# Optimization experiments

Hardware: AMD Instinct MI355X
Metric: run time of the kernel (lower is better)

The kernel has to match this reference:

```python
import jax, jax.numpy as jnp
import numpy as np
import math

B, T, IN, H, OUT, L = 8, 256, 128, 128, 128, 2
MAX_EP_LEN = 10000.0


def _rotate(x, pos, d):
    # rope as in source: repeat(1,1,2) = concat along last dim (not interleave)
    half = jnp.exp(jnp.arange(0, d, 2, dtype=jnp.float32) * (-math.log(MAX_EP_LEN) / d))  # [d/2]
    ang = pos[..., None] * half  # [B,T,d/2]
    sine = jnp.concatenate([jnp.sin(ang), jnp.sin(ang)], axis=-1)
    cos = jnp.concatenate([jnp.cos(ang), jnp.cos(ang)], axis=-1)
    y1, y2 = jnp.split(x, 2, axis=-1)
    x_rot = jnp.concatenate([-y2, y1], axis=-1)
    return x * cos + x_rot * sine


def _layernorm(x, w, b, eps=1e-5):
    m = jnp.mean(x, axis=-1, keepdims=True)
    v = jnp.mean((x - m) ** 2, axis=-1, keepdims=True)
    return (x - m) / jnp.sqrt(v + eps) * w + b


def _block(x, S0, Z0, Wk, Wq, Wv, lw, lb, w1, b1, w2, b2, scw, scb):
    # x: [B,T,F]; S0: [B,F,F]; Z0: [B,F]
    x = _layernorm(x, lw, lb)
    K = jax.nn.elu(x @ Wk.T) + 1.0
    Q = jax.nn.elu(x @ Wq.T) + 1.0
    V = x @ Wv.T
    outer = jnp.einsum('bti,btj->btij', K, V)  # [B,T,F,F]
    S = jnp.clip(jnp.cumsum(outer, axis=1), -1e20, 1e20) + S0[:, None]  # [B,T,F,F]
    Z = jnp.clip(jnp.cumsum(K, axis=1), -1e20, 1e20) + Z0[:, None]      # [B,T,F]
    num = jnp.einsum('bti,btil->btl', Q, S)
    den = jnp.einsum('bti,bti->bt', Q, Z)[..., None] + 1e-5
    out = num / den
    out = jax.nn.relu(jax.nn.relu(out @ w1.T + b1) @ w2.T + b2)  # feed_forward
    out = out + x @ scw.T + scb                                   # residual shortcut
    return out, S[:, -1], Z[:, -1]


def setup_inputs() -> dict:
    key = jax.random.key(0)
    ks = jax.random.split(key, 14)
    s = 0.05
    return {
        'z': jax.random.normal(ks[0], (T, B, IN), jnp.float32),
        'state': jnp.zeros((B, L * (H * H + H) + 1), jnp.float32),
        'Wk': jax.random.normal(ks[1], (L, H, IN), jnp.float32) * s,
        'Wq': jax.random.normal(ks[2], (L, H, IN), jnp.float32) * s,
        'Wv': jax.random.normal(ks[3], (L, H, IN), jnp.float32) * s,
        'ln_w': jnp.ones((L, IN), jnp.float32),
        'ln_b': jnp.zeros((L, IN), jnp.float32),
        'ff_w1': jax.random.normal(ks[4], (L, H, H), jnp.float32) * s,
        'ff_b1': jnp.zeros((L, H), jnp.float32),
        'ff_w2': jax.random.normal(ks[5], (L, H, H), jnp.float32) * s,
        'ff_b2': jnp.zeros((L, H), jnp.float32),
        'sc_w': jax.random.normal(ks[6], (L, H, IN), jnp.float32) * s,
        'sc_b': jnp.zeros((L, H), jnp.float32),
        'unmap_w': jax.random.normal(ks[7], (OUT, H), jnp.float32) * s,
        'unmap_b': jnp.zeros((OUT,), jnp.float32),
    }


def reference(z, state, Wk, Wq, Wv, ln_w, ln_b, ff_w1, ff_b1, ff_w2, ff_b2, sc_w, sc_b, unmap_w, unmap_b):
    x = jnp.transpose(z, (1, 0, 2))  # [B,T,IN]
    ts = state[:, -1]                # [B] timestep counters
    core = state[:, :-1].reshape(B, L, H * H + H)
    pos = ts[:, None] + jnp.arange(T, dtype=jnp.float32)[None, :]  # [B,T]
    x = _rotate(x, pos, IN)  # embedding_type == 'rope'
    new_states = []
    for i in range(L):
        S0 = core[:, i, :H * H].reshape(B, H, H)
        Z0 = core[:, i, H * H:]
        x, Sl, Zl = _block(x, S0, Z0, Wk[i], Wq[i], Wv[i], ln_w[i], ln_b[i],
                           ff_w1[i], ff_b1[i], ff_w2[i], ff_b2[i], sc_w[i], sc_b[i])
        new_states.append(jnp.concatenate([Sl.reshape(B, -1), Zl], axis=-1))
    y = x @ unmap_w.T + unmap_b
    st = jnp.concatenate([jnp.stack(new_states, axis=1).reshape(B, -1), (ts + T)[:, None]], axis=-1)
    return jnp.transpose(y, (1, 0, 2)), st
```

## Files before the change

### kernel.cpp

```cpp
#include <hip/hip_runtime.h>
#include <math.h>

#define Bn 8
#define Tn 256
#define COREn 16512
#define SDn   33025

typedef __attribute__((ext_vector_type(8))) short short8;
typedef __attribute__((ext_vector_type(4))) short short4v;
typedef __attribute__((ext_vector_type(4))) float floatx4;

#define MFMA16(a,b,c) __builtin_amdgcn_mfma_f32_16x16x32_bf16(a,b,c,0,0,0)

static __device__ __forceinline__ unsigned short f2bf(float f) {
  unsigned int u = __float_as_uint(f);
  return (unsigned short)((u + 0x7FFFu + ((u >> 16) & 1u)) >> 16);
}
static __device__ __forceinline__ float bf2f(unsigned short h) {
  return __uint_as_float((unsigned int)h << 16);
}
static __device__ __forceinline__ short8 ldwfrag(const float* p) {
  float4 a = *(const float4*)p;
  float4 b = *(const float4*)(p + 4);
  short8 r;
  r[0] = (short)f2bf(a.x); r[1] = (short)f2bf(a.y);
  r[2] = (short)f2bf(a.z); r[3] = (short)f2bf(a.w);
  r[4] = (short)f2bf(b.x); r[5] = (short)f2bf(b.y);
  r[6] = (short)f2bf(b.z); r[7] = (short)f2bf(b.w);
  return r;
}
static __device__ __forceinline__ void ld8(const float* p, float* v) {
  float4 a = *(const float4*)p, b = *(const float4*)(p + 4);
  v[0]=a.x; v[1]=a.y; v[2]=a.z; v[3]=a.w; v[4]=b.x; v[5]=b.y; v[6]=b.z; v[7]=b.w;
}

static __device__ __forceinline__ void proj_epilogue(
    int by, int g0, int b, int t0l, int n0, int n1, int quad,
    floatx4 acc0, floatx4 acc1,
    unsigned short* __restrict__ Kb, unsigned short* __restrict__ Kt,
    unsigned short* __restrict__ Qb, unsigned short* __restrict__ Vt,
    unsigned short* __restrict__ skipb, const float* __restrict__ scb) {
  if (by == 0) {
    short4v kt0, kt1;
#pragma unroll
    for (int j = 0; j < 4; j++) {
      int row = quad * 4 + j;
      float e0 = acc0[j] > 0.f ? acc0[j] + 1.f : expf(acc0[j]);
      float e1 = acc1[j] > 0.f ? acc1[j] + 1.f : expf(acc1[j]);
      Kb[(size_t)(g0 + row) * 128 + n0] = f2bf(e0);
      Kb[(size_t)(g0 + row) * 128 + n1] = f2bf(e1);
      kt0[j] = (short)f2bf(e0); kt1[j] = (short)f2bf(e1);
    }
    *(short4v*)(Kt + (size_t)(b * 128 + n0) * 256 + t0l + quad * 4) = kt0;
    *(short4v*)(Kt + (size_t)(b * 128 + n1) * 256 + t0l + quad * 4) = kt1;
  } else if (by == 1) {
#pragma unroll
    for (int j = 0; j < 4; j++) {
      int row = quad * 4 + j;
      float e0 = acc0[j] > 0.f ? acc0[j] + 1.f : expf(acc0[j]);
      float e1 = acc1[j] > 0.f ? acc1[j] + 1.f : expf(acc1[j]);
      Qb[(size_t)(g0 + row) * 128 + n0] = f2bf(e0);
      Qb[(size_t)(g0 + row) * 128 + n1] = f2bf(e1);
    }
  } else if (by == 2) {
    short4v v0, v1;
#pragma unroll
    for (int j = 0; j < 4; j++) { v0[j] = (short)f2bf(acc0[j]); v1[j] = (short)f2bf(acc1[j]); }
    *(short4v*)(Vt + (size_t)(b * 128 + n0) * 256 + t0l + quad * 4) = v0;
    *(short4v*)(Vt + (size_t)(b * 128 + n1) * 256 + t0l + quad * 4) = v1;
  } else {
    float sb0 = scb[n0], sb1 = scb[n1];
#pragma unroll
    for (int j = 0; j < 4; j++) {
      int row = quad * 4 + j;
      skipb[(size_t)(g0 + row) * 128 + n0] = f2bf(acc0[j] + sb0);
      skipb[(size_t)(g0 + row) * 128 + n1] = f2bf(acc1[j] + sb1);
    }
  }
}

__global__ __launch_bounds__(256) void prep_kernel(
    const float* __restrict__ z, const float* __restrict__ state,
    const float* __restrict__ Wk, const float* __restrict__ Wq,
    const float* __restrict__ Wv, const float* __restrict__ scw,
    const float* __restrict__ lnw, const float* __restrict__ lnb,
    const float* __restrict__ scb,
    unsigned short* __restrict__ Kb0, unsigned short* __restrict__ Qb0,
    unsigned short* __restrict__ Kt0, unsigned short* __restrict__ Vt0,
    unsigned short* __restrict__ skip0, unsigned short* __restrict__ S0t) {
  const int tid = threadIdx.x, bx = blockIdx.x;
  if (bx < 512) {
    __shared__ unsigned short xs[16][136];
    const int lane = tid & 63, wv = tid >> 6, lm = lane & 15, quad = lane >> 4;
    const int tile = bx >> 2, by = bx & 3;
    const int g0 = tile * 16;
    const int r = tid >> 4, c0 = (tid & 15) * 8;
    const int g = g0 + r, b = g >> 8, t = g & 255;
    float v[8], pv[8];
    const float* zr = z + ((size_t)t * Bn + b) * 128;
    ld8(zr + c0, v);
    ld8(zr + (c0 ^ 64), pv);
    float pos = state[(size_t)b * SDn + SDn - 1] + (float)t;
#pragma unroll
    for (int i = 0; i < 8; i++) {
      int jj = (c0 + i) & 63;
      float ang = pos * expf((float)jj * -0.14391156831212787f);
      float sn = sinf(ang), cs = cosf(ang);
      v[i] = (c0 < 64) ? (v[i] * cs - pv[i] * sn) : (v[i] * cs + pv[i] * sn);
    }
    float sm = 0.f, sq = 0.f;
#pragma unroll
    for (int i = 0; i < 8; i++) { sm += v[i]; sq += v[i] * v[i]; }
    for (int d = 8; d; d >>= 1) { sm += __shfl_xor(sm, d, 16); sq += __shfl_xor(sq, d, 16); }
    float mean = sm * (1.f / 128.f);
    float rstd = rsqrtf(sq * (1.f / 128.f) - mean * mean + 1e-5f);
    short8 xv;
#pragma unroll
    for (int i = 0; i < 8; i++)
      xv[i] = (short)f2bf((v[i] - mean) * rstd * lnw[c0 + i] + lnb[c0 + i]);
    *(short8*)&xs[r][c0] = xv;
    __syncthreads();

    const float* W = by == 0 ? Wk : by == 1 ? Wq : by == 2 ? Wv : scw;
    const int bb = g0 >> 8, t0l = g0 & 255;
    const int n0 = wv * 32 + lm, n1 = n0 + 16;
    floatx4 a0 = {0.f,0.f,0.f,0.f}, a1 = {0.f,0.f,0.f,0.f};
#pragma unroll
    for (int kc = 0; kc < 4; kc++) {
      short8 a  = *(const short8*)&xs[lm][kc * 32 + quad * 8];
      short8 bA = ldwfrag(W + (size_t)n0 * 128 + kc * 32 + quad * 8);
      short8 bB = ldwfrag(W + (size_t)n1 * 128 + kc * 32 + quad * 8);
      a0 = MFMA16(a, bA, a0);
      a1 = MFMA16(a, bB, a1);
    }
    proj_epilogue(by, g0, bb, t0l, n0, n1, quad, a0, a1,
                  Kb0, Kt0, Qb0, Vt0, skip0, scb);
  } else {
    __shared__ float tl[32][33];
    const int id = bx - 512, b = id >> 1, l = id & 1;
    const float* src = state + (size_t)b * SDn + (size_t)l * COREn;
    unsigned short* dst = S0t + (size_t)(l * 8 + b) * 16384;
    const int r = tid >> 3, c4 = (tid & 7) * 4;
#pragma unroll
    for (int tI = 0; tI < 4; tI++)
      for (int tJ = 0; tJ < 4; tJ++) {
        int i0 = tI * 32, j0 = tJ * 32;
#pragma unroll
        for (int q = 0; q < 4; q++)
          tl[r][c4 + q] = src[(size_t)(i0 + r) * 128 + j0 + c4 + q];
        __syncthreads();
        short4v o;
#pragma unroll
        for (int q = 0; q < 4; q++) o[q] = (short)f2bf(tl[c4 + q][r]);
        *(short4v*)(dst + (size_t)(j0 + r) * 128 + i0 + c4) = o;
        __syncthreads();
      }
  }
}

static __device__ void state_upd(
    int tid, int idx, int l,
    const unsigned short* __restrict__ Kt, const unsigned short* __restrict__ Vt,
    const float* __restrict__ state, float* __restrict__ st_out) {
  const int lane = tid & 63, wv = tid >> 6, lm = lane & 15, quad = lane >> 4;
  const int b = idx >> 4, sub = idx & 15;
  const int i0 = (sub >> 1) * 16, j0 = (sub & 1) * 64;
  const size_t sb = (size_t)b * SDn + (size_t)l * COREn;
  floatx4 acc = {0.f, 0.f, 0.f, 0.f};
#pragma unroll
  for (int kc = 0; kc < 8; kc++) {
    short8 ka = *(const short8*)(Kt + (size_t)(b * 128 + i0 + lm) * 256 + kc * 32 + quad * 8);
    short8 vb = *(const short8*)(Vt + (size_t)(b * 128 + j0 + wv * 16 + lm) * 256 + kc * 32 + quad * 8);
    acc = MFMA16(ka, vb, acc);
  }
#pragma unroll
  for (int j = 0; j < 4; j++) {
    size_t off = sb + (size_t)(i0 + quad * 4 + j) * 128 + j0 + wv * 16 + lm;
    st_out[off] = acc[j] + state[off];
  }
  if (j0 == 0) {
    if (tid < 128) {
      int i = tid >> 3, seg = tid & 7;
      const unsigned short* kr = Kt + (size_t)(b * 128 + i0 + i) * 256 + seg * 32;
      float zs = 0.f;
#pragma unroll
      for (int x = 0; x < 4; x++) {
        short8 kv = *(const short8*)(kr + x * 8);
#pragma unroll
        for (int y = 0; y < 8; y++) zs += bf2f((unsigned short)kv[y]);
      }
      for (int d = 4; d; d >>= 1) zs += __shfl_xor(zs, d, 8);
      if (seg == 0) {
        size_t zo = sb + 16384 + i0 + i;
        st_out[zo] = zs + state[zo];
      }
    }
    if (sub == 0 && tid == 0 && l == 0)
      st_out[(size_t)b * SDn + SDn - 1] = state[(size_t)b * SDn + SDn - 1] + 256.f;
  }
}

__global__ __launch_bounds__(256) void attn_kernel(
    const unsigned short* __restrict__ Kb, const unsigned short* __restrict__ Qb,
    const unsigned short* __restrict__ Vt, const unsigned short* __restrict__ Kt,
    const unsigned short* __restrict__ S0tl, const float* __restrict__ state,
    unsigned short* __restrict__ attnb, float* __restrict__ st_out, int l) {
  const int tid = threadIdx.x, bx = blockIdx.x;
  const int lane = tid & 63, wv = tid >> 6, lm = lane & 15, quad = lane >> 4;
  if (bx < 256) {
    __shared__ unsigned short xs[16][136];
    __shared__ unsigned short Ssc[4][16][40];
    __shared__ float Obuf[4][16][68];
    __shared__ float Z0s[128];
    __shared__ float denw[4][16];
    __shared__ float denz[16];
    __shared__ float dinv[16];

    const int tile = bx >> 1, half = bx & 1;
    const int b = tile >> 4, rt = tile & 15, t0 = rt * 16;
    const size_t sb = (size_t)b * SDn + (size_t)l * COREn;
    { int r = tid >> 4, c = (tid & 15) * 8;
      *(short8*)&xs[r][c] = *(const short8*)(Qb + (size_t)(b * 256 + t0 + r) * 128 + c); }
    if (tid < 128) Z0s[tid] = state[sb + 16384 + tid];
    __syncthreads();

    { int r = tid >> 4, c = (tid & 15) * 8;
      float qz = 0.f;
#pragma unroll
      for (int i = 0; i < 8; i++) qz += bf2f(xs[r][c + i]) * Z0s[c + i];
      for (int d = 8; d; d >>= 1) qz += __shfl_xor(qz, d, 16);
      if ((tid & 15) == 0) denz[r] = qz; }

    floatx4 oacc[4];
#pragma unroll
    for (int jt = 0; jt < 4; jt++) oacc[jt] = floatx4{0.f, 0.f, 0.f, 0.f};
    float dacc[4] = {0.f, 0.f, 0.f, 0.f};

    const int nch = rt / 2 + 1;
    for (int c = wv; c < nch; c += 4) {
      const int kb = c * 32;
      short8 vfr[4];
#pragma unroll
      for (int jt = 0; jt < 4; jt++)
        vfr[jt] = *(const short8*)(Vt + (size_t)(b * 128 + half * 64 + jt * 16 + lm) * 256 + kb + quad * 8);
      floatx4 s0 = {0.f,0.f,0.f,0.f}, s1 = {0.f,0.f,0.f,0.f};
#pragma unroll
      for (int kc = 0; kc < 4; kc++) {
        short8 a  = *(const short8*)&xs[lm][kc * 32 + quad * 8];
        short8 k0 = *(const short8*)(Kb + (size_t)(b * 256 + kb + lm) * 128 + kc * 32 + quad * 8);
        short8 k1 = *(const short8*)(Kb + (size_t)(b * 256 + kb + 16 + lm) * 128 + kc * 32 + quad * 8);
        s0 = MFMA16(a, k0, s0);
        s1 = MFMA16(a, k1, s1);
      }
      const int tau0 = kb + lm, tau1 = kb + 16 + lm;
#pragma unroll
      for (int j = 0; j < 4; j++) {
        int m = t0 + quad * 4 + j;
        float v0 = (tau0 <= m) ? s0[j] : 0.f;
        float v1 = (tau1 <= m) ? s1[j] : 0.f;
        dacc[j] += v0 + v1;
        Ssc[wv][quad * 4 + j][lm]      = f2bf(v0);
        Ssc[wv][quad * 4 + j][16 + lm] = f2bf(v1);
      }
      short8 sa = *(const short8*)&Ssc[wv][lm][quad * 8];
#pragma unroll
      for (int jt = 0; jt < 4; jt++)
        oacc[jt] = MFMA16(sa, vfr[jt], oacc[jt]);
    }

    { short8 aq = *(const short8*)&xs[lm][wv * 32 + quad * 8];
#pragma unroll
      for (int jt = 0; jt < 4; jt++) {
        short8 vb = *(const short8*)(S0tl + (size_t)b * 16384 +
                        (size_t)(half * 64 + jt * 16 + lm) * 128 + wv * 32 + quad * 8);
        oacc[jt] = MFMA16(aq, vb, oacc[jt]);
      } }

#pragma unroll
    for (int j = 0; j < 4; j++)
      for (int d = 8; d; d >>= 1) dacc[j] += __shfl_xor(dacc[j], d, 16);
    if (lm == 0) {
#pragma unroll
      for (int j = 0; j < 4; j++) denw[wv][quad * 4 + j] = dacc[j];
    }
#pragma unroll
    for (int jt = 0; jt < 4; jt++)
#pragma unroll
      for (int j = 0; j < 4; j++)
        Obuf[wv][quad * 4 + j][jt * 16 + lm] = oacc[jt][j];
    __syncthreads();
    if (tid < 16)
      dinv[tid] = 1.f / (denz[tid] + denw[0][tid] + denw[1][tid]
                         + denw[2][tid] + denw[3][tid] + 1e-5f);
    __syncthreads();
    { int r = tid >> 4, c = (tid & 15) * 4;
      float di = dinv[r];
      short4v ov;
#pragma unroll
      for (int q = 0; q < 4; q++) {
        float o = Obuf[0][r][c + q] + Obuf[1][r][c + q]
                + Obuf[2][r][c + q] + Obuf[3][r][c + q];
        ov[q] = (short)f2bf(o * di);
      }
      *(short4v*)(attnb + (size_t)(b * 256 + t0 + r) * 128 + half * 64 + c) = ov; }
  } else {
    state_upd(tid, bx - 256, l, Kt, Vt, state, st_out);
  }
}

__global__ __launch_bounds__(256) void ffln_kernel(
    const unsigned short* __restrict__ attnb, const unsigned short* __restrict__ skipb,
    const float* __restrict__ w1, const float* __restrict__ b1,
    const float* __restrict__ w2, const float* __restrict__ b2,
    const float* __restrict__ lnw1, const float* __restrict__ lnb1,
    unsigned short* __restrict__ xln1) {
  __shared__ unsigned short xa[16][136];
  __shared__ unsigned short hs[16][136];
  __shared__ float os[16][132];
  const int tid = threadIdx.x, g0 = blockIdx.x * 16;
  const int lane = tid & 63, wv = tid >> 6, lm = lane & 15, quad = lane >> 4;
  const int n0 = wv * 32 + lm, n1 = n0 + 16;

  short8 w1A[4], w1B[4], w2A[4], w2B[4];
#pragma unroll
  for (int kc = 0; kc < 4; kc++) {
    w1A[kc] = ldwfrag(w1 + (size_t)n0 * 128 + kc * 32 + quad * 8);
    w1B[kc] = ldwfrag(w1 + (size_t)n1 * 128 + kc * 32 + quad * 8);
    w2A[kc] = ldwfrag(w2 + (size_t)n0 * 128 + kc * 32 + quad * 8);
    w2B[kc] = ldwfrag(w2 + (size_t)n1 * 128 + kc * 32 + quad * 8);
  }
  float bi10 = b1[n0], bi11 = b1[n1], bi20 = b2[n0], bi21 = b2[n1];
  float sk0[4], sk1[4];
#pragma unroll
  for (int j = 0; j < 4; j++) {
    sk0[j] = bf2f(skipb[(size_t)(g0 + quad * 4 + j) * 128 + n0]);
    sk1[j] = bf2f(skipb[(size_t)(g0 + quad * 4 + j) * 128 + n1]);
  }
  { int r = tid >> 4, c = (tid & 15) * 8;
    *(short8*)&xa[r][c] = *(const short8*)(attnb + (size_t)(g0 + r) * 128 + c); }
  __syncthreads();

  { floatx4 a0 = {0.f,0.f,0.f,0.f}, a1 = {0.f,0.f,0.f,0.f};
#pragma unroll
    for (int kc = 0; kc < 4; kc++) {
      short8 a = *(const short8*)&xa[lm][kc * 32 + quad * 8];
      a0 = MFMA16(a, w1A[kc], a0);
      a1 = MFMA16(a, w1B[kc], a1);
    }
#pragma unroll
    for (int j = 0; j < 4; j++) {
      int row = quad * 4 + j;
      hs[row][n0] = f2bf(fmaxf(a0[j] + bi10, 0.f));
      hs[row][n1] = f2bf(fmaxf(a1[j] + bi11, 0.f));
    } }
  __syncthreads();
  { floatx4 a0 = {0.f,0.f,0.f,0.f}, a1 = {0.f,0.f,0.f,0.f};
#pragma unroll
    for (int kc = 0; kc < 4; kc++) {
      short8 a = *(const short8*)&hs[lm][kc * 32 + quad * 8];
      a0 = MFMA16(a, w2A[kc], a0);
      a1 = MFMA16(a, w2B[kc], a1);
    }
#pragma unroll
    for (int j = 0; j < 4; j++) {
      int row = quad * 4 + j;
      os[row][n0] = fmaxf(a0[j] + bi20, 0.f) + sk0[j];
      os[row][n1] = fmaxf(a1[j] + bi21, 0.f) + sk1[j];
    } }
  __syncthreads();
  { int r = tid >> 4, c0 = (tid & 15) * 8;
    float v[8];
#pragma unroll
    for (int i = 0; i < 8; i++) v[i] = os[r][c0 + i];
    float sm = 0.f, sq = 0.f;
#pragma unroll
    for (int i = 0; i < 8; i++) { sm += v[i]; sq += v[i] * v[i]; }
    for (int d = 8; d; d >>= 1) { sm += __shfl_xor(sm, d, 16); sq += __shfl_xor(sq, d, 16); }
    float mean = sm * (1.f / 128.f);
    float rstd = rsqrtf(sq * (1.f / 128.f) - mean * mean + 1e-5f);
    short8 xv;
#pragma unroll
    for (int i = 0; i < 8; i++)
      xv[i] = (short)f2bf((v[i] - mean) * rstd * lnw1[c0 + i] + lnb1[c0 + i]);
    *(short8*)(xln1 + (size_t)(g0 + r) * 128 + c0) = xv; }
}

__global__ __launch_bounds__(256) void proj1_kernel(
    const unsigned short* __restrict__ xln1,
    const float* __restrict__ Wk, const float* __restrict__ Wq,
    const float* __restrict__ Wv, const float* __restrict__ scw,
    const float* __restrict__ scb,
    unsigned short* __restrict__ Kb1, unsigned short* __restrict__ Qb1,
    unsigned short* __restrict__ Kt1, unsigned short* __restrict__ Vt1,
    unsigned short* __restrict__ skip1) {
  __shared__ unsigned short xs[16][136];
  const int tid = threadIdx.x, bx = blockIdx.x;
  const int lane = tid & 63, wv = tid >> 6, lm = lane & 15, quad = lane >> 4;
  const int tile = bx >> 2, by = bx & 3;
  const int g0 = tile * 16;
  { int r = tid >> 4, c = (tid & 15) * 8;
    *(short8*)&xs[r][c] = *(const short8*)(xln1 + (size_t)(g0 + r) * 128 + c); }
  __syncthreads();
  const float* W = by == 0 ? Wk : by == 1 ? Wq : by == 2 ? Wv : scw;
  const int bb = g0 >> 8, t0l = g0 & 255;
  const int n0 = wv * 32 + lm, n1 = n0 + 16;
  floatx4 a0 = {0.f,0.f,0.f,0.f}, a1 = {0.f,0.f,0.f,0.f};
#pragma unroll
  for (int kc = 0; kc < 4; kc++) {
    short8 a  = *(const short8*)&xs[lm][kc * 32 + quad * 8];
    short8 bA = ldwfrag(W + (size_t)n0 * 128 + kc * 32 + quad * 8);
    short8 bB = ldwfrag(W + (size_t)n1 * 128 + kc * 32 + quad * 8);
    a0 = MFMA16(a, bA, a0);
    a1 = MFMA16(a, bB, a1);
  }
  proj_epilogue(by, g0, bb, t0l, n0, n1, quad, a0, a1,
                Kb1, Kt1, Qb1, Vt1, skip1, scb);
}

__global__ __launch_bounds__(256) void ffu_kernel(
    const unsigned short* __restrict__ attnb, const unsigned short* __restrict__ skipb,
    const float* __restrict__ w1, const float* __restrict__ b1,
    const float* __restrict__ w2, const float* __restrict__ b2,
    const float* __restrict__ unw, const float* __restrict__ unb,
    float* __restrict__ yout) {
  __shared__ unsigned short xa[16][136];
  __shared__ unsigned short hs[16][136];
  const int tid = threadIdx.x, g0 = blockIdx.x * 16;
  const int lane = tid & 63, wv = tid >> 6, lm = lane & 15, quad = lane >> 4;
  const int n0 = wv * 32 + lm, n1 = n0 + 16;

  short8 w1A[4], w1B[4], w2A[4], w2B[4];
#pragma unroll
  for (int kc = 0; kc < 4; kc++) {
    w1A[kc] = ldwfrag(w1 + (size_t)n0 * 128 + kc * 32 + quad * 8);
    w1B[kc] = ldwfrag(w1 + (size_t)n1 * 128 + kc * 32 + quad * 8);
    w2A[kc] = ldwfrag(w2 + (size_t)n0 * 128 + kc * 32 + quad * 8);
    w2B[kc] = ldwfrag(w2 + (size_t)n1 * 128 + kc * 32 + quad * 8);
  }
  float bi10 = b1[n0], bi11 = b1[n1], bi20 = b2[n0], bi21 = b2[n1];
  float sk0[4], sk1[4];
#pragma unroll
  for (int j = 0; j < 4; j++) {
    sk0[j] = bf2f(skipb[(size_t)(g0 + quad * 4 + j) * 128 + n0]);
    sk1[j] = bf2f(skipb[(size_t)(g0 + quad * 4 + j) * 128 + n1]);
  }
  { int r = tid >> 4, c = (tid & 15) * 8;
    *(short8*)&xa[r][c] = *(const short8*)(attnb + (size_t)(g0 + r) * 128 + c); }
  __syncthreads();

  { floatx4 a0 = {0.f,0.f,0.f,0.f}, a1 = {0.f,0.f,0.f,0.f};
#pragma unroll
    for (int kc = 0; kc < 4; kc++) {
      short8 a = *(const short8*)&xa[lm][kc * 32 + quad * 8];
      a0 = MFMA16(a, w1A[kc], a0);
      a1 = MFMA16(a, w1B[kc], a1);
    }
#pragma unroll
    for (int j = 0; j < 4; j++) {
      int row = quad * 4 + j;
      hs[row][n0] = f2bf(fmaxf(a0[j] + bi10, 0.f));
      hs[row][n1] = f2bf(fmaxf(a1[j] + bi11, 0.f));
    } }
  __syncthreads();
  short8 uA[4], uB[4];
#pragma unroll
  for (int kc = 0; kc < 4; kc++) {
    uA[kc] = ldwfrag(unw + (size_t)n0 * 128 + kc * 32 + quad * 8);
    uB[kc] = ldwfrag(unw + (size_t)n1 * 128 + kc * 32 + quad * 8);
  }
  float o0[4], o1[4];
  { floatx4 a0 = {0.f,0.f,0.f,0.f}, a1 = {0.f,0.f,0.f,0.f};
#pragma unroll
    for (int kc = 0; kc < 4; kc++) {
      short8 a = *(const short8*)&hs[lm][kc * 32 + quad * 8];
      a0 = MFMA16(a, w2A[kc], a0);
      a1 = MFMA16(a, w2B[kc], a1);
    }
#pragma unroll
    for (int j = 0; j < 4; j++) {
      o0[j] = fmaxf(a0[j] + bi20, 0.f) + sk0[j];
      o1[j] = fmaxf(a1[j] + bi21, 0.f) + sk1[j];
    } }
  __syncthreads();
#pragma unroll
  for (int j = 0; j < 4; j++) {
    int row = quad * 4 + j;
    hs[row][n0] = f2bf(o0[j]);
    hs[row][n1] = f2bf(o1[j]);
  }
  __syncthreads();
  { floatx4 a0 = {0.f,0.f,0.f,0.f}, a1 = {0.f,0.f,0.f,0.f};
#pragma unroll
    for (int kc = 0; kc < 4; kc++) {
      short8 a = *(const short8*)&hs[lm][kc * 32 + quad * 8];
      a0 = MFMA16(a, uA[kc], a0);
      a1 = MFMA16(a, uB[kc], a1);
    }
    float u0 = unb[n0], u1 = unb[n1];
#pragma unroll
    for (int j = 0; j < 4; j++) {
      int gg = g0 + quad * 4 + j;
      int bb = gg >> 8, tq = gg & 255;
      yout[(size_t)(tq * Bn + bb) * 128 + n0] = a0[j] + u0;
      yout[(size_t)(tq * Bn + bb) * 128 + n1] = a1[j] + u1;
    } }
}

extern "C" void kernel_launch(void* const* d_in, const int* in_sizes, int n_in,
                              void* d_out, int out_size, void* d_ws, size_t ws_size,
                              hipStream_t stream) {
  const float* z       = (const float*)d_in[0];
  const float* state   = (const float*)d_in[1];
  const float* Wk      = (const float*)d_in[2];
  const float* Wq      = (const float*)d_in[3];
  const float* Wv      = (const float*)d_in[4];
  const float* ln_w    = (const float*)d_in[5];
  const float* ln_b    = (const float*)d_in[6];
  const float* ff_w1   = (const float*)d_in[7];
  const float* ff_b1   = (const float*)d_in[8];
  const float* ff_w2   = (const float*)d_in[9];
  const float* ff_b2   = (const float*)d_in[10];
  const float* sc_w    = (const float*)d_in[11];
  const float* sc_b    = (const float*)d_in[12];
  const float* unmap_w = (const float*)d_in[13];
  const float* unmap_b = (const float*)d_in[14];

  float* y_out  = (float*)d_out;
  float* st_out = y_out + (size_t)Tn * Bn * 128;

  const size_t E = 262144;
  unsigned short* Kb0  = (unsigned short*)d_ws;
  unsigned short* Qb0  = Kb0 + E;
  unsigned short* Kt0  = Qb0 + E;
  unsigned short* Vt0  = Kt0 + E;
  unsigned short* Kb1  = Vt0 + E;
  unsigned short* Qb1  = Kb1 + E;
  unsigned short* Kt1  = Qb1 + E;
  unsigned short* Vt1  = Kt1 + E;
  unsigned short* skip0 = Vt1 + E;
  unsigned short* skip1 = skip0 + E;
  unsigned short* attnb = skip1 + E;
  unsigned short* xln1  = attnb + E;
  unsigned short* S0t   = xln1 + E;

  prep_kernel<<<528, 256, 0, stream>>>(
      z, state, Wk, Wq, Wv, sc_w, ln_w, ln_b, sc_b,
      Kb0, Qb0, Kt0, Vt0, skip0, S0t);

  attn_kernel<<<384, 256, 0, stream>>>(
      Kb0, Qb0, Vt0, Kt0, S0t, state, attnb, st_out, 0);

  ffln_kernel<<<128, 256, 0, stream>>>(
      attnb, skip0, ff_w1, ff_b1, ff_w2, ff_b2,
      ln_w + 128, ln_b + 128, xln1);

  proj1_kernel<<<512, 256, 0, stream>>>(
      xln1, Wk + 16384, Wq + 16384, Wv + 16384, sc_w + 16384, sc_b + 128,
      Kb1, Qb1, Kt1, Vt1, skip1);

  attn_kernel<<<384, 256, 0, stream>>>(
      Kb1, Qb1, Vt1, Kt1, S0t + (size_t)8 * 16384, state, attnb, st_out, 1);

  ffu_kernel<<<128, 256, 0, stream>>>(
      attnb, skip1, ff_w1 + 16384, ff_b1 + 128, ff_w2 + 16384, ff_b2 + 128,
      unmap_w, unmap_b, y_out);
}
```

Baseline: 130.4 us.

## Fuse FF/LN with layer-1 projection, hoist loads, and prewarm weights in L2

Merges the ffln and proj1 kernels into a single ffproj kernel. The layer-1 LayerNorm output now stays in shared memory instead of round-tripping through a global xln1 buffer, and one launch is removed. The attention, prep and state-update kernels issue all K/V/S0/weight fragment loads up front into registers so memory latency overlaps with compute. The attention loop is unrolled to two fixed chunks per wave. Extra prep blocks read the layer-1 and FF weights to warm the L2 cache, and launch_bounds(256,1) is added; in exchange ffproj has only 128 blocks doing four projections each, which lowers parallelism, and register use rises.

```diff
diff --git a/kernel.cpp b/kernel.cpp
--- a/kernel.cpp
+++ b/kernel.cpp
@@ -79,15 +79,18 @@
   }
 }
 
-__global__ __launch_bounds__(256) void prep_kernel(
+__global__ __launch_bounds__(256, 1) void prep_kernel(
     const float* __restrict__ z, const float* __restrict__ state,
     const float* __restrict__ Wk, const float* __restrict__ Wq,
     const float* __restrict__ Wv, const float* __restrict__ scw,
     const float* __restrict__ lnw, const float* __restrict__ lnb,
     const float* __restrict__ scb,
+    const float* __restrict__ w1all, const float* __restrict__ w2all,
+    const float* __restrict__ unw,
     unsigned short* __restrict__ Kb0, unsigned short* __restrict__ Qb0,
     unsigned short* __restrict__ Kt0, unsigned short* __restrict__ Vt0,
-    unsigned short* __restrict__ skip0, unsigned short* __restrict__ S0t) {
+    unsigned short* __restrict__ skip0, unsigned short* __restrict__ S0t,
+    float* __restrict__ warm_sink) {
   const int tid = threadIdx.x, bx = blockIdx.x;
   if (bx < 512) {
     __shared__ unsigned short xs[16][136];
@@ -96,11 +99,21 @@
     const int g0 = tile * 16;
     const int r = tid >> 4, c0 = (tid & 15) * 8;
     const int g = g0 + r, b = g >> 8, t = g & 255;
+    const int n0 = wv * 32 + lm, n1 = n0 + 16;
+
     float v[8], pv[8];
     const float* zr = z + ((size_t)t * Bn + b) * 128;
     ld8(zr + c0, v);
     ld8(zr + (c0 ^ 64), pv);
+    const float* W = by == 0 ? Wk : by == 1 ? Wq : by == 2 ? Wv : scw;
+    short8 bA[4], bB[4];
+#pragma unroll
+    for (int kc = 0; kc < 4; kc++) {
+      bA[kc] = ldwfrag(W + (size_t)n0 * 128 + kc * 32 + quad * 8);
+      bB[kc] = ldwfrag(W + (size_t)n1 * 128 + kc * 32 + quad * 8);
+    }
     float pos = state[(size_t)b * SDn + SDn - 1] + (float)t;
+
 #pragma unroll
     for (int i = 0; i < 8; i++) {
       int jj = (c0 + i) & 63;
@@ -121,21 +134,17 @@
     *(short8*)&xs[r][c0] = xv;
     __syncthreads();
 
-    const float* W = by == 0 ? Wk : by == 1 ? Wq : by == 2 ? Wv : scw;
     const int bb = g0 >> 8, t0l = g0 & 255;
-    const int n0 = wv * 32 + lm, n1 = n0 + 16;
     floatx4 a0 = {0.f,0.f,0.f,0.f}, a1 = {0.f,0.f,0.f,0.f};
 #pragma unroll
     for (int kc = 0; kc < 4; kc++) {
-      short8 a  = *(const short8*)&xs[lm][kc * 32 + quad * 8];
-      short8 bA = ldwfrag(W + (size_t)n0 * 128 + kc * 32 + quad * 8);
-      short8 bB = ldwfrag(W + (size_t)n1 * 128 + kc * 32 + quad * 8);
-      a0 = MFMA16(a, bA, a0);
-      a1 = MFMA16(a, bB, a1);
+      short8 a = *(const short8*)&xs[lm][kc * 32 + quad * 8];
+      a0 = MFMA16(a, bA[kc], a0);
+      a1 = MFMA16(a, bB[kc], a1);
     }
     proj_epilogue(by, g0, bb, t0l, n0, n1, quad, a0, a1,
                   Kb0, Kt0, Qb0, Vt0, skip0, scb);
-  } else {
+  } else if (bx < 528) {
     __shared__ float tl[32][33];
     const int id = bx - 512, b = id >> 1, l = id & 1;
     const float* src = state + (size_t)b * SDn + (size_t)l * COREn;
@@ -155,6 +164,17 @@
         *(short4v*)(dst + (size_t)(j0 + r) * 128 + i0 + c4) = o;
         __syncthreads();
       }
+  } else {
+    const int wb = bx - 528;
+    const float* ptrs[9] = { w1all, w1all + 16384, w2all, w2all + 16384, unw,
+                             Wk + 16384, Wq + 16384, Wv + 16384, scw + 16384 };
+    float acc = 0.f;
+#pragma unroll
+    for (int i = 0; i < 9; i++) {
+      float4 vv = ((const float4*)ptrs[i])[wb * 256 + tid];
+      acc += vv.x + vv.y + vv.z + vv.w;
+    }
+    if (acc == 1234567.89f) warm_sink[0] = acc;
   }
 }
 
@@ -166,13 +186,15 @@
   const int b = idx >> 4, sub = idx & 15;
   const int i0 = (sub >> 1) * 16, j0 = (sub & 1) * 64;
   const size_t sb = (size_t)b * SDn + (size_t)l * COREn;
+  short8 ka[8], vb[8];
+#pragma unroll
+  for (int kc = 0; kc < 8; kc++) {
+    ka[kc] = *(const short8*)(Kt + (size_t)(b * 128 + i0 + lm) * 256 + kc * 32 + quad * 8);
+    vb[kc] = *(const short8*)(Vt + (size_t)(b * 128 + j0 + wv * 16 + lm) * 256 + kc * 32 + quad * 8);
+  }
   floatx4 acc = {0.f, 0.f, 0.f, 0.f};
 #pragma unroll
-  for (int kc = 0; kc < 8; kc++) {
-    short8 ka = *(const short8*)(Kt + (size_t)(b * 128 + i0 + lm) * 256 + kc * 32 + quad * 8);
-    short8 vb = *(const short8*)(Vt + (size_t)(b * 128 + j0 + wv * 16 + lm) * 256 + kc * 32 + quad * 8);
-    acc = MFMA16(ka, vb, acc);
-  }
+  for (int kc = 0; kc < 8; kc++) acc = MFMA16(ka[kc], vb[kc], acc);
 #pragma unroll
   for (int j = 0; j < 4; j++) {
     size_t off = sb + (size_t)(i0 + quad * 4 + j) * 128 + j0 + wv * 16 + lm;
@@ -200,7 +222,7 @@
   }
 }
 
-__global__ __launch_bounds__(256) void attn_kernel(
+__global__ __launch_bounds__(256, 1) void attn_kernel(
     const unsigned short* __restrict__ Kb, const unsigned short* __restrict__ Qb,
     const unsigned short* __restrict__ Vt, const unsigned short* __restrict__ Kt,
     const unsigned short* __restrict__ S0tl, const float* __restrict__ state,
@@ -219,15 +241,38 @@
     const int tile = bx >> 1, half = bx & 1;
     const int b = tile >> 4, rt = tile & 15, t0 = rt * 16;
     const size_t sb = (size_t)b * SDn + (size_t)l * COREn;
-    { int r = tid >> 4, c = (tid & 15) * 8;
-      *(short8*)&xs[r][c] = *(const short8*)(Qb + (size_t)(b * 256 + t0 + r) * 128 + c); }
-    if (tid < 128) Z0s[tid] = state[sb + 16384 + tid];
+
+    const int r = tid >> 4, cQ = (tid & 15) * 8;
+    short8 qrow = *(const short8*)(Qb + (size_t)(b * 256 + t0 + r) * 128 + cQ);
+    float z0v = (tid < 128) ? state[sb + 16384 + tid] : 0.f;
+
+    const int nch = rt / 2 + 1;
+    const bool hasA = (wv < nch), hasB = (wv + 4 < nch);
+    const int kbA = (hasA ? wv : nch - 1) * 32;
+    const int kbB = (hasB ? wv + 4 : nch - 1) * 32;
+    short8 KA[8], KB[8], VA[4], VB[4], SF[4];
+#pragma unroll
+    for (int kc = 0; kc < 4; kc++) {
+      KA[kc]     = *(const short8*)(Kb + (size_t)(b * 256 + kbA + lm) * 128 + kc * 32 + quad * 8);
+      KA[4 + kc] = *(const short8*)(Kb + (size_t)(b * 256 + kbA + 16 + lm) * 128 + kc * 32 + quad * 8);
+      KB[kc]     = *(const short8*)(Kb + (size_t)(b * 256 + kbB + lm) * 128 + kc * 32 + quad * 8);
+      KB[4 + kc] = *(const short8*)(Kb + (size_t)(b * 256 + kbB + 16 + lm) * 128 + kc * 32 + quad * 8);
+    }
+#pragma unroll
+    for (int jt = 0; jt < 4; jt++) {
+      VA[jt] = *(const short8*)(Vt + (size_t)(b * 128 + half * 64 + jt * 16 + lm) * 256 + kbA + quad * 8);
+      VB[jt] = *(const short8*)(Vt + (size_t)(b * 128 + half * 64 + jt * 16 + lm) * 256 + kbB + quad * 8);
+      SF[jt] = *(const short8*)(S0tl + (size_t)b * 16384 +
+                    (size_t)(half * 64 + jt * 16 + lm) * 128 + wv * 32 + quad * 8);
+    }
+
+    *(short8*)&xs[r][cQ] = qrow;
+    if (tid < 128) Z0s[tid] = z0v;
     __syncthreads();
 
-    { int r = tid >> 4, c = (tid & 15) * 8;
-      float qz = 0.f;
-#pragma unroll
-      for (int i = 0; i < 8; i++) qz += bf2f(xs[r][c + i]) * Z0s[c + i];
+    { float qz = 0.f;
+#pragma unroll
+      for (int i = 0; i < 8; i++) qz += bf2f(xs[r][cQ + i]) * Z0s[cQ + i];
       for (int d = 8; d; d >>= 1) qz += __shfl_xor(qz, d, 16);
       if ((tid & 15) == 0) denz[r] = qz; }
 
@@ -236,45 +281,53 @@
     for (int jt = 0; jt < 4; jt++) oacc[jt] = floatx4{0.f, 0.f, 0.f, 0.f};
     float dacc[4] = {0.f, 0.f, 0.f, 0.f};
 
-    const int nch = rt / 2 + 1;
-    for (int c = wv; c < nch; c += 4) {
-      const int kb = c * 32;
-      short8 vfr[4];
-#pragma unroll
-      for (int jt = 0; jt < 4; jt++)
-        vfr[jt] = *(const short8*)(Vt + (size_t)(b * 128 + half * 64 + jt * 16 + lm) * 256 + kb + quad * 8);
+    {
       floatx4 s0 = {0.f,0.f,0.f,0.f}, s1 = {0.f,0.f,0.f,0.f};
 #pragma unroll
       for (int kc = 0; kc < 4; kc++) {
-        short8 a  = *(const short8*)&xs[lm][kc * 32 + quad * 8];
-        short8 k0 = *(const short8*)(Kb + (size_t)(b * 256 + kb + lm) * 128 + kc * 32 + quad * 8);
-        short8 k1 = *(const short8*)(Kb + (size_t)(b * 256 + kb + 16 + lm) * 128 + kc * 32 + quad * 8);
-        s0 = MFMA16(a, k0, s0);
-        s1 = MFMA16(a, k1, s1);
-      }
-      const int tau0 = kb + lm, tau1 = kb + 16 + lm;
+        short8 a = *(const short8*)&xs[lm][kc * 32 + quad * 8];
+        s0 = MFMA16(a, KA[kc], s0);
+        s1 = MFMA16(a, KA[4 + kc], s1);
+      }
+      const int tau0 = kbA + lm, tau1 = kbA + 16 + lm;
 #pragma unroll
       for (int j = 0; j < 4; j++) {
         int m = t0 + quad * 4 + j;
-        float v0 = (tau0 <= m) ? s0[j] : 0.f;
-        float v1 = (tau1 <= m) ? s1[j] : 0.f;
+        float v0 = (hasA && tau0 <= m) ? s0[j] : 0.f;
+        float v1 = (hasA && tau1 <= m) ? s1[j] : 0.f;
         dacc[j] += v0 + v1;
         Ssc[wv][quad * 4 + j][lm]      = f2bf(v0);
         Ssc[wv][quad * 4 + j][16 + lm] = f2bf(v1);
       }
       short8 sa = *(const short8*)&Ssc[wv][lm][quad * 8];
 #pragma unroll
-      for (int jt = 0; jt < 4; jt++)
-        oacc[jt] = MFMA16(sa, vfr[jt], oacc[jt]);
-    }
-
+      for (int jt = 0; jt < 4; jt++) oacc[jt] = MFMA16(sa, VA[jt], oacc[jt]);
+    }
+    {
+      floatx4 s0 = {0.f,0.f,0.f,0.f}, s1 = {0.f,0.f,0.f,0.f};
+#pragma unroll
+      for (int kc = 0; kc < 4; kc++) {
+        short8 a = *(const short8*)&xs[lm][kc * 32 + quad * 8];
+        s0 = MFMA16(a, KB[kc], s0);
+        s1 = MFMA16(a, KB[4 + kc], s1);
+      }
+      const int tau0 = kbB + lm, tau1 = kbB + 16 + lm;
+#pragma unroll
+      for (int j = 0; j < 4; j++) {
+        int m = t0 + quad * 4 + j;
+        float v0 = (hasB && tau0 <= m) ? s0[j] : 0.f;
+        float v1 = (hasB && tau1 <= m) ? s1[j] : 0.f;
+        dacc[j] += v0 + v1;
+        Ssc[wv][quad * 4 + j][lm]      = f2bf(v0);
+        Ssc[wv][quad * 4 + j][16 + lm] = f2bf(v1);
+      }
+      short8 sa = *(const short8*)&Ssc[wv][lm][quad * 8];
+#pragma unroll
+      for (int jt = 0; jt < 4; jt++) oacc[jt] = MFMA16(sa, VB[jt], oacc[jt]);
+    }
     { short8 aq = *(const short8*)&xs[lm][wv * 32 + quad * 8];
 #pragma unroll
-      for (int jt = 0; jt < 4; jt++) {
-        short8 vb = *(const short8*)(S0tl + (size_t)b * 16384 +
-                        (size_t)(half * 64 + jt * 16 + lm) * 128 + wv * 32 + quad * 8);
-        oacc[jt] = MFMA16(aq, vb, oacc[jt]);
-      } }
+      for (int jt = 0; jt < 4; jt++) oacc[jt] = MFMA16(aq, SF[jt], oacc[jt]); }
 
 #pragma unroll
     for (int j = 0; j < 4; j++)
@@ -293,29 +346,35 @@
       dinv[tid] = 1.f / (denz[tid] + denw[0][tid] + denw[1][tid]
                          + denw[2][tid] + denw[3][tid] + 1e-5f);
     __syncthreads();
-    { int r = tid >> 4, c = (tid & 15) * 4;
-      float di = dinv[r];
+    { int rr = tid >> 4, c = (tid & 15) * 4;
+      float di = dinv[rr];
       short4v ov;
 #pragma unroll
       for (int q = 0; q < 4; q++) {
-        float o = Obuf[0][r][c + q] + Obuf[1][r][c + q]
-                + Obuf[2][r][c + q] + Obuf[3][r][c + q];
+        float o = Obuf[0][rr][c + q] + Obuf[1][rr][c + q]
+                + Obuf[2][rr][c + q] + Obuf[3][rr][c + q];
         ov[q] = (short)f2bf(o * di);
       }
-      *(short4v*)(attnb + (size_t)(b * 256 + t0 + r) * 128 + half * 64 + c) = ov; }
+      *(short4v*)(attnb + (size_t)(b * 256 + t0 + rr) * 128 + half * 64 + c) = ov; }
   } else {
     state_upd(tid, bx - 256, l, Kt, Vt, state, st_out);
   }
 }
 
-__global__ __launch_bounds__(256) void ffln_kernel(
+__global__ __launch_bounds__(256, 1) void ffproj_kernel(
     const unsigned short* __restrict__ attnb, const unsigned short* __restrict__ skipb,
     const float* __restrict__ w1, const float* __restrict__ b1,
     const float* __restrict__ w2, const float* __restrict__ b2,
     const float* __restrict__ lnw1, const float* __restrict__ lnb1,
-    unsigned short* __restrict__ xln1) {
+    const float* __restrict__ Wk1, const float* __restrict__ Wq1,
+    const float* __restrict__ Wv1, const float* __restrict__ scw1,
+    const float* __restrict__ scb1,
+    unsigned short* __restrict__ Kb1, unsigned short* __restrict__ Qb1,
+    unsigned short* __restrict__ Kt1, unsigned short* __restrict__ Vt1,
+    unsigned short* __restrict__ skip1) {
   __shared__ unsigned short xa[16][136];
   __shared__ unsigned short hs[16][136];
+  __shared__ unsigned short xsl[16][136];
   __shared__ float os[16][132];
   const int tid = threadIdx.x, g0 = blockIdx.x * 16;
   const int lane = tid & 63, wv = tid >> 6, lm = lane & 15, quad = lane >> 4;
@@ -382,42 +441,31 @@
 #pragma unroll
     for (int i = 0; i < 8; i++)
       xv[i] = (short)f2bf((v[i] - mean) * rstd * lnw1[c0 + i] + lnb1[c0 + i]);
-    *(short8*)(xln1 + (size_t)(g0 + r) * 128 + c0) = xv; }
-}
-
-__global__ __launch_bounds__(256) void proj1_kernel(
-    const unsigned short* __restrict__ xln1,
-    const float* __restrict__ Wk, const float* __restrict__ Wq,
-    const float* __restrict__ Wv, const float* __restrict__ scw,
-    const float* __restrict__ scb,
-    unsigned short* __restrict__ Kb1, unsigned short* __restrict__ Qb1,
-    unsigned short* __restrict__ Kt1, unsigned short* __restrict__ Vt1,
-    unsigned short* __restrict__ skip1) {
-  __shared__ unsigned short xs[16][136];
-  const int tid = threadIdx.x, bx = blockIdx.x;
-  const int lane = tid & 63, wv = tid >> 6, lm = lane & 15, quad = lane >> 4;
-  const int tile = bx >> 2, by = bx & 3;
-  const int g0 = tile * 16;
-  { int r = tid >> 4, c = (tid & 15) * 8;
-    *(short8*)&xs[r][c] = *(const short8*)(xln1 + (size_t)(g0 + r) * 128 + c); }
-  __syncthreads();
-  const float* W = by == 0 ? Wk : by == 1 ? Wq : by == 2 ? Wv : scw;
+    *(short8*)&xsl[r][c0] = xv; }
+  __syncthreads();
   const int bb = g0 >> 8, t0l = g0 & 255;
-  const int n0 = wv * 32 + lm, n1 = n0 + 16;
-  floatx4 a0 = {0.f,0.f,0.f,0.f}, a1 = {0.f,0.f,0.f,0.f};
-#pragma unroll
-  for (int kc = 0; kc < 4; kc++) {
-    short8 a  = *(const short8*)&xs[lm][kc * 32 + quad * 8];
-    short8 bA = ldwfrag(W + (size_t)n0 * 128 + kc * 32 + quad * 8);
-    short8 bB = ldwfrag(W + (size_t)n1 * 128 + kc * 32 + quad * 8);
-    a0 = MFMA16(a, bA, a0);
-    a1 = MFMA16(a, bB, a1);
-  }
-  proj_epilogue(by, g0, bb, t0l, n0, n1, quad, a0, a1,
-                Kb1, Kt1, Qb1, Vt1, skip1, scb);
-}
-
-__global__ __launch_bounds__(256) void ffu_kernel(
+#pragma unroll
+  for (int by = 0; by < 4; by++) {
+    const float* W = by == 0 ? Wk1 : by == 1 ? Wq1 : by == 2 ? Wv1 : scw1;
+    short8 bA[4], bB[4];
+#pragma unroll
+    for (int kc = 0; kc < 4; kc++) {
+      bA[kc] = ldwfrag(W + (size_t)n0 * 128 + kc * 32 + quad * 8);
+      bB[kc] = ldwfrag(W + (size_t)n1 * 128 + kc * 32 + quad * 8);
+    }
+    floatx4 a0 = {0.f,0.f,0.f,0.f}, a1 = {0.f,0.f,0.f,0.f};
+#pragma unroll
+    for (int kc = 0; kc < 4; kc++) {
+      short8 a = *(const short8*)&xsl[lm][kc * 32 + quad * 8];
+      a0 = MFMA16(a, bA[kc], a0);
+      a1 = MFMA16(a, bB[kc], a1);
+    }
+    proj_epilogue(by, g0, bb, t0l, n0, n1, quad, a0, a1,
+                  Kb1, Kt1, Qb1, Vt1, skip1, scb1);
+  }
+}
+
+__global__ __launch_bounds__(256, 1) void ffu_kernel(
     const unsigned short* __restrict__ attnb, const unsigned short* __restrict__ skipb,
     const float* __restrict__ w1, const float* __restrict__ b1,
     const float* __restrict__ w2, const float* __restrict__ b2,
@@ -429,15 +477,18 @@
   const int lane = tid & 63, wv = tid >> 6, lm = lane & 15, quad = lane >> 4;
   const int n0 = wv * 32 + lm, n1 = n0 + 16;
 
-  short8 w1A[4], w1B[4], w2A[4], w2B[4];
+  short8 w1A[4], w1B[4], w2A[4], w2B[4], uA[4], uB[4];
 #pragma unroll
   for (int kc = 0; kc < 4; kc++) {
     w1A[kc] = ldwfrag(w1 + (size_t)n0 * 128 + kc * 32 + quad * 8);
     w1B[kc] = ldwfrag(w1 + (size_t)n1 * 128 + kc * 32 + quad * 8);
     w2A[kc] = ldwfrag(w2 + (size_t)n0 * 128 + kc * 32 + quad * 8);
     w2B[kc] = ldwfrag(w2 + (size_t)n1 * 128 + kc * 32 + quad * 8);
+    uA[kc]  = ldwfrag(unw + (size_t)n0 * 128 + kc * 32 + quad * 8);
+    uB[kc]  = ldwfrag(unw + (size_t)n1 * 128 + kc * 32 + quad * 8);
   }
   float bi10 = b1[n0], bi11 = b1[n1], bi20 = b2[n0], bi21 = b2[n1];
+  float u0b = unb[n0], u1b = unb[n1];
   float sk0[4], sk1[4];
 #pragma unroll
   for (int j = 0; j < 4; j++) {
@@ -462,12 +513,6 @@
       hs[row][n1] = f2bf(fmaxf(a1[j] + bi11, 0.f));
     } }
   __syncthreads();
-  short8 uA[4], uB[4];
-#pragma unroll
-  for (int kc = 0; kc < 4; kc++) {
-    uA[kc] = ldwfrag(unw + (size_t)n0 * 128 + kc * 32 + quad * 8);
-    uB[kc] = ldwfrag(unw + (size_t)n1 * 128 + kc * 32 + quad * 8);
-  }
   float o0[4], o1[4];
   { floatx4 a0 = {0.f,0.f,0.f,0.f}, a1 = {0.f,0.f,0.f,0.f};
 #pragma unroll
@@ -496,13 +541,12 @@
       a0 = MFMA16(a, uA[kc], a0);
       a1 = MFMA16(a, uB[kc], a1);
     }
-    float u0 = unb[n0], u1 = unb[n1];
 #pragma unroll
     for (int j = 0; j < 4; j++) {
       int gg = g0 + quad * 4 + j;
       int bb = gg >> 8, tq = gg & 255;
-      yout[(size_t)(tq * Bn + bb) * 128 + n0] = a0[j] + u0;
-      yout[(size_t)(tq * Bn + bb) * 128 + n1] = a1[j] + u1;
+      yout[(size_t)(tq * Bn + bb) * 128 + n0] = a0[j] + u0b;
+      yout[(size_t)(tq * Bn + bb) * 128 + n1] = a1[j] + u1b;
     } }
 }
 
@@ -540,22 +584,21 @@
   unsigned short* skip0 = Vt1 + E;
   unsigned short* skip1 = skip0 + E;
   unsigned short* attnb = skip1 + E;
-  unsigned short* xln1  = attnb + E;
-  unsigned short* S0t   = xln1 + E;
-
-  prep_kernel<<<528, 256, 0, stream>>>(
+  unsigned short* S0t   = attnb + E;
+  float* warm_sink = (float*)(S0t + (size_t)2 * 8 * 16384);
+
+  prep_kernel<<<544, 256, 0, stream>>>(
       z, state, Wk, Wq, Wv, sc_w, ln_w, ln_b, sc_b,
-      Kb0, Qb0, Kt0, Vt0, skip0, S0t);
+      ff_w1, ff_w2, unmap_w,
+      Kb0, Qb0, Kt0, Vt0, skip0, S0t, warm_sink);
 
   attn_kernel<<<384, 256, 0, stream>>>(
       Kb0, Qb0, Vt0, Kt0, S0t, state, attnb, st_out, 0);
 
-  ffln_kernel<<<128, 256, 0, stream>>>(
+  ffproj_kernel<<<128, 256, 0, stream>>>(
       attnb, skip0, ff_w1, ff_b1, ff_w2, ff_b2,
-      ln_w + 128, ln_b + 128, xln1);
-
-  proj1_kernel<<<512, 256, 0, stream>>>(
-      xln1, Wk + 16384, Wq + 16384, Wv + 16384, sc_w + 16384, sc_b + 128,
+      ln_w + 128, ln_b + 128,
+      Wk + 16384, Wq + 16384, Wv + 16384, sc_w + 16384, sc_b + 128,
       Kb1, Qb1, Kt1, Vt1, skip1);
 
   attn_kernel<<<384, 256, 0, stream>>>(
```

Measured after the change: 133.8 us. 1.03x slower.
